# Kernel tuning notes

Measured on AMD Instinct MI355X. Metric: run time of the kernel, lower is better.

Reference implementation:

```python
import jax, jax.numpy as jnp
import numpy as np

B, T, E, H = 2, 2048, 1024, 16
DV = E // H
EPS = 1e-5

def _layernorm(x, g, b):
    m = jnp.mean(x, axis=-1, keepdims=True)
    v = jnp.mean((x - m) ** 2, axis=-1, keepdims=True)
    return (x - m) * jax.lax.rsqrt(v + EPS) * g + b

def setup_inputs() -> dict:
    key = jax.random.key(0)
    ks = jax.random.split(key, 10)
    s = lambda fan_in: 1.0 / np.sqrt(fan_in)
    return {
        "x": jax.random.normal(ks[0], (B, T, E), jnp.float32),
        "wq": jax.random.normal(ks[1], (H, E, DV), jnp.float32) * s(E),
        "wk": jax.random.normal(ks[2], (H, E, DV), jnp.float32) * s(E),
        "wv": jax.random.normal(ks[3], (H, E, DV), jnp.float32) * s(E),
        "w_proj": jax.random.normal(ks[4], (E, E), jnp.float32) * s(E),
        "b_proj": jnp.zeros((E,), jnp.float32),
        "w1": jax.random.normal(ks[5], (E, 4 * E), jnp.float32) * s(E),
        "b1": jnp.zeros((4 * E,), jnp.float32),
        "w2": jax.random.normal(ks[6], (4 * E, E), jnp.float32) * s(4 * E),
        "b2": jnp.zeros((E,), jnp.float32),
        "g1": jnp.ones((E,), jnp.float32),
        "be1": jnp.zeros((E,), jnp.float32),
        "g2": jnp.ones((E,), jnp.float32),
        "be2": jnp.zeros((E,), jnp.float32),
    }

def reference(x, wq, wk, wv, w_proj, b_proj, w1, b1, w2, b2, g1, be1, g2, be2):
    Bc, Tc, C = x.shape
    # --- masked multi-head self-attention on pre-LN input ---
    h = _layernorm(x, g1, be1)
    q = jnp.einsum('bte,hed->bhtd', h, wq)
    k = jnp.einsum('bte,hed->bhtd', h, wk)
    v = jnp.einsum('bte,hed->bhtd', h, wv)
    # NOTE: original scales by C**-0.5 where C = full embed dim (not head dim)
    scores = jnp.einsum('bhtd,bhsd->bhts', q, k) * (C ** -0.5)
    causal = jnp.tril(jnp.ones((Tc, Tc), bool))
    scores = jnp.where(causal, scores, jnp.float32(-jnp.inf))
    probs = jax.nn.softmax(scores, axis=-1)  # dropout is identity in eval
    attn = jnp.einsum('bhts,bhsd->bhtd', probs, v)
    attn = attn.transpose(0, 2, 1, 3).reshape(Bc, Tc, C)
    x = x + (attn @ w_proj + b_proj)
    # --- feed-forward ---
    h2 = _layernorm(x, g2, be2)
    ff = jax.nn.relu(h2 @ w1 + b1) @ w2 + b2
    return x + ff
```

## Files before the change

### kernel.cpp

```cpp
#include <hip/hip_runtime.h>
#include <hip/hip_bf16.h>

typedef __bf16 bf16x8 __attribute__((ext_vector_type(8)));
typedef __bf16 bf16x4 __attribute__((ext_vector_type(4)));
typedef float f32x4 __attribute__((ext_vector_type(4)));

#define T_SEQ 2048
#define EMB 1024
#define NH 16
#define DV 64

__device__ __forceinline__ void gload16(const __bf16* g, __bf16* l) {
    __builtin_amdgcn_global_load_lds(
        (const __attribute__((address_space(1))) unsigned int*)g,
        (__attribute__((address_space(3))) unsigned int*)l, 16, 0, 0);
}

__global__ void transpose_cvt(const float* __restrict__ src, __bf16* __restrict__ dst,
                              int R, int C, long src_bstride, long dst_bstride, float scale) {
    __shared__ float tile[32][33];
    const int b = blockIdx.z;
    const float* s = src + (long)b * src_bstride;
    __bf16* d = dst + (long)b * dst_bstride;
    const int c0 = blockIdx.x * 32, r0 = blockIdx.y * 32;
    #pragma unroll
    for (int i = threadIdx.y; i < 32; i += 8)
        tile[i][threadIdx.x] = s[(long)(r0 + i) * C + c0 + threadIdx.x];
    __syncthreads();
    #pragma unroll
    for (int i = threadIdx.y; i < 32; i += 8)
        d[(long)(c0 + i) * R + r0 + threadIdx.x] = (__bf16)(tile[threadIdx.x][i] * scale);
}

__global__ void vt_transpose(const __bf16* __restrict__ qkv, __bf16* __restrict__ Vt) {
    __shared__ __bf16 tile[64][72];
    const int bh = blockIdx.y, b = bh >> 4, h = bh & 15;
    const int t0 = blockIdx.x * 64;
    const __bf16* src = qkv + (long)b * T_SEQ * 3072 + 2048 + h * 64;
    const int tt = threadIdx.x >> 3, seg = threadIdx.x & 7;
    #pragma unroll
    for (int half = 0; half < 2; half++) {
        const int t = half * 32 + tt;
        bf16x8 v = *reinterpret_cast<const bf16x8*>(src + (long)(t0 + t) * 3072 + seg * 8);
        *reinterpret_cast<bf16x8*>(&tile[t][seg * 8]) = v;
    }
    __syncthreads();
    __bf16* dst = Vt + (long)bh * 64 * T_SEQ + t0;
    #pragma unroll
    for (int half = 0; half < 2; half++) {
        const int d = half * 32 + tt;
        bf16x8 v;
        #pragma unroll
        for (int i = 0; i < 8; i++) v[i] = tile[seg * 8 + i][d];
        *reinterpret_cast<bf16x8*>(dst + (long)d * T_SEQ + seg * 8) = v;
    }
}

__global__ void ln_kernel(const float* __restrict__ x, const float* __restrict__ g,
                          const float* __restrict__ be, __bf16* __restrict__ out) {
    const int row = blockIdx.x;
    const float4 xv = reinterpret_cast<const float4*>(x + (long)row * EMB)[threadIdx.x];
    float s = xv.x + xv.y + xv.z + xv.w;
    float sq = xv.x * xv.x + xv.y * xv.y + xv.z * xv.z + xv.w * xv.w;
    #pragma unroll
    for (int off = 32; off; off >>= 1) { s += __shfl_down(s, off); sq += __shfl_down(sq, off); }
    __shared__ float red[8];
    const int w = threadIdx.x >> 6, lane = threadIdx.x & 63;
    if (lane == 0) { red[w] = s; red[4 + w] = sq; }
    __syncthreads();
    if (threadIdx.x == 0) {
        float st = red[0] + red[1] + red[2] + red[3];
        float sqt = red[4] + red[5] + red[6] + red[7];
        float mean = st * (1.0f / EMB);
        float var = sqt * (1.0f / EMB) - mean * mean;
        red[0] = mean; red[1] = rsqrtf(var + 1e-5f);
    }
    __syncthreads();
    const float mean = red[0], rstd = red[1];
    const float4 gv = reinterpret_cast<const float4*>(g)[threadIdx.x];
    const float4 bv = reinterpret_cast<const float4*>(be)[threadIdx.x];
    bf16x4 o;
    o[0] = (__bf16)((xv.x - mean) * rstd * gv.x + bv.x);
    o[1] = (__bf16)((xv.y - mean) * rstd * gv.y + bv.y);
    o[2] = (__bf16)((xv.z - mean) * rstd * gv.z + bv.z);
    o[3] = (__bf16)((xv.w - mean) * rstd * gv.w + bv.w);
    *reinterpret_cast<bf16x4*>(out + (long)row * EMB + threadIdx.x * 4) = o;
}

template <int BN, int OUT_BF16, int RELU, int HAS_BIAS, int HAS_RES>
__global__ __launch_bounds__(256)
void gemm_nt(const __bf16* __restrict__ A, const __bf16* __restrict__ BT,
             const float* __restrict__ bias, const float* __restrict__ res,
             void* __restrict__ outp, int M, int N, int K) {
    constexpr int NFN = BN / 32;
    __shared__ __align__(16) __bf16 As[128 * 64];
    __shared__ __align__(16) __bf16 Bs[BN * 64];
    const int t = threadIdx.x;
    const int w = t >> 6, lane = t & 63;
    const int wm = (w >> 1) * 64, wn = (w & 1) * (BN / 2);
    const int m0 = blockIdx.y * 128, n0 = blockIdx.x * BN;
    const int rA = lane & 15, kA = (lane >> 4) * 8;
    const int swzr = (rA & 7) * 8;
    const int srow = t >> 3;
    const int chunk = t & 7;
    const int schunk = chunk ^ (srow & 7);

    const __bf16* Ab = A + (long)(m0 + srow) * K + schunk * 8;
    const __bf16* Bb = BT + (long)(n0 + srow) * K + schunk * 8;
    __bf16* Asw = As + srow * 64 + chunk * 8;
    __bf16* Bsw = Bs + srow * 64 + chunk * 8;

    f32x4 acc[4][NFN] = {};
    for (int k0 = 0; k0 < K; k0 += 64) {
        #pragma unroll
        for (int i = 0; i < 4; i++)
            gload16(Ab + (long)(32 * i) * K + k0, Asw + 32 * i * 64);
        #pragma unroll
        for (int i = 0; i < BN / 32; i++)
            gload16(Bb + (long)(32 * i) * K + k0, Bsw + 32 * i * 64);
        __syncthreads();
        #pragma unroll
        for (int kk = 0; kk < 2; kk++) {
            bf16x8 af[4], bfr[NFN];
            #pragma unroll
            for (int m = 0; m < 4; m++)
                af[m] = *reinterpret_cast<const bf16x8*>(
                    As + (wm + m * 16 + rA) * 64 + ((kk * 32 + kA) ^ swzr));
            #pragma unroll
            for (int n = 0; n < NFN; n++)
                bfr[n] = *reinterpret_cast<const bf16x8*>(
                    Bs + (wn + n * 16 + rA) * 64 + ((kk * 32 + kA) ^ swzr));
            #pragma unroll
            for (int m = 0; m < 4; m++)
                #pragma unroll
                for (int n = 0; n < NFN; n++)
                    acc[m][n] = __builtin_amdgcn_mfma_f32_16x16x32_bf16(af[m], bfr[n], acc[m][n], 0, 0, 0);
        }
        __syncthreads();
    }
    const int rl = (lane >> 4) * 4, cl = lane & 15;
    #pragma unroll
    for (int m = 0; m < 4; m++) {
        #pragma unroll
        for (int n = 0; n < NFN; n++) {
            const int gc = n0 + wn + n * 16 + cl;
            float bval = 0.0f;
            if (HAS_BIAS) bval = bias[gc];
            #pragma unroll
            for (int r = 0; r < 4; r++) {
                const int gr = m0 + wm + m * 16 + rl + r;
                float v = acc[m][n][r] + bval;
                if (HAS_RES) v += res[(long)gr * N + gc];
                if (RELU) v = fmaxf(v, 0.0f);
                if (OUT_BF16) ((__bf16*)outp)[(long)gr * N + gc] = (__bf16)v;
                else          ((float*)outp)[(long)gr * N + gc] = v;
            }
        }
    }
}

template <int MASKED>
__device__ __forceinline__ void attn_compute(
    const char* __restrict__ Kl, const char* __restrict__ Vl,
    __bf16 (*__restrict__ PsW)[72],
    const bf16x8 (&qf)[2][2], const bf16x8& ones,
    f32x4 (&o)[2][4], f32x4 (&l5)[2], float (&mr)[2][4],
    int kv0, int rA, int g, int rl, int qw)
{
    const int swz = (rA & 7) << 4;
    bf16x8 kf[4][2];
    #pragma unroll
    for (int c = 0; c < 4; c++)
        #pragma unroll
        for (int kc = 0; kc < 2; kc++)
            kf[c][kc] = *reinterpret_cast<const bf16x8*>(
                Kl + (c * 16 + rA) * 128 + ((kc * 64 + g * 16) ^ swz));
    f32x4 sa[2][4];
    __builtin_amdgcn_s_setprio(1);
    #pragma unroll
    for (int rt = 0; rt < 2; rt++)
        #pragma unroll
        for (int c = 0; c < 4; c++) {
            f32x4 acc = {};
            acc = __builtin_amdgcn_mfma_f32_16x16x32_bf16(qf[rt][0], kf[c][0], acc, 0, 0, 0);
            acc = __builtin_amdgcn_mfma_f32_16x16x32_bf16(qf[rt][1], kf[c][1], acc, 0, 0, 0);
            sa[rt][c] = acc;
        }
    __builtin_amdgcn_s_setprio(0);
    #pragma unroll
    for (int rt = 0; rt < 2; rt++) {
        #pragma unroll
        for (int r = 0; r < 4; r++) {
            float s0 = sa[rt][0][r], s1 = sa[rt][1][r], s2 = sa[rt][2][r], s3 = sa[rt][3][r];
            if (MASKED) {
                const int gr = qw + rt * 16 + rl + r;
                if (kv0 + rA > gr)      s0 = -__builtin_inff();
                if (kv0 + 16 + rA > gr) s1 = -__builtin_inff();
                if (kv0 + 32 + rA > gr) s2 = -__builtin_inff();
                if (kv0 + 48 + rA > gr) s3 = -__builtin_inff();
            }
            float tm = fmaxf(fmaxf(s0, s1), fmaxf(s2, s3));
            #pragma unroll
            for (int msk = 1; msk < 16; msk <<= 1) tm = fmaxf(tm, __shfl_xor(tm, msk));
            const float mo = mr[rt][r];
            float mu = mo;
            if (__any(tm > mo + 8.0f)) {
                const float mn = fmaxf(mo, tm);
                mr[rt][r] = mn;
                const float sc = __expf(mo - mn);
                #pragma unroll
                for (int n = 0; n < 4; n++) o[rt][n][r] *= sc;
                l5[rt][r] *= sc;
                mu = mn;
            }
            const float p0 = __expf(s0 - mu);
            const float p1 = __expf(s1 - mu);
            const float p2 = __expf(s2 - mu);
            const float p3 = __expf(s3 - mu);
            const int prow = rt * 16 + rl + r;
            PsW[prow][rA]      = (__bf16)p0;
            PsW[prow][16 + rA] = (__bf16)p1;
            PsW[prow][32 + rA] = (__bf16)p2;
            PsW[prow][48 + rA] = (__bf16)p3;
        }
    }
    asm volatile("s_waitcnt lgkmcnt(0)" ::: "memory");

    bf16x8 ap[2][2];
    #pragma unroll
    for (int rt = 0; rt < 2; rt++)
        #pragma unroll
        for (int ks = 0; ks < 2; ks++)
            ap[rt][ks] = *reinterpret_cast<const bf16x8*>(&PsW[rt * 16 + rA][ks * 32 + g * 8]);
    __builtin_amdgcn_s_setprio(1);
    #pragma unroll
    for (int ks = 0; ks < 2; ks++) {
        #pragma unroll
        for (int rt = 0; rt < 2; rt++)
            l5[rt] = __builtin_amdgcn_mfma_f32_16x16x32_bf16(ap[rt][ks], ones, l5[rt], 0, 0, 0);
        #pragma unroll
        for (int n = 0; n < 4; n++) {
            bf16x8 bv = *reinterpret_cast<const bf16x8*>(
                Vl + (n * 16 + rA) * 128 + ((ks * 64 + g * 16) ^ swz));
            #pragma unroll
            for (int rt = 0; rt < 2; rt++)
                o[rt][n] = __builtin_amdgcn_mfma_f32_16x16x32_bf16(ap[rt][ks], bv, o[rt][n], 0, 0, 0);
        }
    }
    __builtin_amdgcn_s_setprio(0);
}

__global__ __launch_bounds__(256)
void attn_kernel(const __bf16* __restrict__ qkv, const __bf16* __restrict__ Vt,
                 __bf16* __restrict__ attn) {
    __shared__ __bf16 Ks[2][64 * 64];
    __shared__ __bf16 Vs[2][64 * 64];
    __shared__ __bf16 Ps[4][32][72];

    const int bid = (int)blockIdx.x;
    const int xcd = bid & 7, s = bid >> 3;
    const int slot = s >> 5, c = s & 31;
    const int bh = xcd * 4 + slot * 2 + (c >> 4);
    const int t16 = c & 15;
    const int qtile = slot ? t16 : 15 - t16;
    const int b = bh >> 4, h = bh & 15;
    const int q0 = qtile * 128;
    const int w = threadIdx.x >> 6, lane = threadIdx.x & 63;
    const int qw = q0 + w * 32;
    const int rA = lane & 15, g = lane >> 4, rl = g * 4;
    const int srow8 = lane >> 3;
    const int scol = (lane & 7) * 16;
    const int wcol = scol ^ (srow8 << 4);

    const char* qb = (const char*)(qkv + (long)b * T_SEQ * 3072 + h * 64);
    const char* kb = qb + 2048;
    const char* vtb = (const char*)(Vt + (long)bh * 64 * T_SEQ);

    bf16x8 qf[2][2];
    #pragma unroll
    for (int rt = 0; rt < 2; rt++)
        #pragma unroll
        for (int kc = 0; kc < 2; kc++)
            qf[rt][kc] = *reinterpret_cast<const bf16x8*>(
                qb + (long)(qw + rt * 16 + rA) * 6144 + kc * 64 + g * 16);

    bf16x8 ones;
    #pragma unroll
    for (int i = 0; i < 8; i++) ones[i] = (__bf16)1.0f;

    f32x4 o[2][4] = {};
    f32x4 l5[2] = {};
    float mr[2][4];
    #pragma unroll
    for (int rt = 0; rt < 2; rt++)
        #pragma unroll
        for (int r = 0; r < 4; r++) mr[rt][r] = -__builtin_inff();

    const int nsteps = q0 / 64 + 2;
    const int t_avail = qw + 32;
    const int isK = (w < 2);
    const int r0 = (w & 1) * 32 + srow8;

    bf16x8 stg[4];
    auto issue = [&](int kv0) {
        if (isK) {
            #pragma unroll
            for (int i = 0; i < 4; i++)
                stg[i] = *reinterpret_cast<const bf16x8*>(kb + (long)(kv0 + r0 + i * 8) * 6144 + scol);
        } else {
            #pragma unroll
            for (int i = 0; i < 4; i++)
                stg[i] = *reinterpret_cast<const bf16x8*>(vtb + (long)(r0 + i * 8) * 4096 + kv0 * 2 + scol);
        }
    };
    auto lwrite = [&](int buf) {
        char* base = isK ? (char*)Ks[buf] : (char*)Vs[buf];
        #pragma unroll
        for (int i = 0; i < 4; i++)
            *reinterpret_cast<bf16x8*>(base + (r0 + i * 8) * 128 + wcol) = stg[i];
    };

    issue(0);
    lwrite(0);
    __syncthreads();

    for (int t = 0; t < nsteps; ++t) {
        const int kv0 = t * 64, cur = t & 1;
        const bool has_next = (t + 1 < nsteps);
        if (has_next) issue(kv0 + 64);
        if (kv0 < t_avail) {
            if (kv0 + 64 <= qw)
                attn_compute<0>((const char*)Ks[cur], (const char*)Vs[cur], Ps[w],
                                qf, ones, o, l5, mr, kv0, rA, g, rl, qw);
            else
                attn_compute<1>((const char*)Ks[cur], (const char*)Vs[cur], Ps[w],
                                qf, ones, o, l5, mr, kv0, rA, g, rl, qw);
        }
        if (has_next) lwrite(cur ^ 1);
        __syncthreads();
    }

    #pragma unroll
    for (int rt = 0; rt < 2; rt++)
        #pragma unroll
        for (int n = 0; n < 4; n++)
            #pragma unroll
            for (int r = 0; r < 4; r++) {
                const int gr = qw + rt * 16 + rl + r;
                attn[(long)(b * T_SEQ + gr) * EMB + h * 64 + n * 16 + rA] =
                    (__bf16)(o[rt][n][r] / l5[rt][r]);
            }
}

extern "C" void kernel_launch(void* const* d_in, const int* in_sizes, int n_in,
                              void* d_out, int out_size, void* d_ws, size_t ws_size,
                              hipStream_t stream) {
    const float* x      = (const float*)d_in[0];
    const float* wq     = (const float*)d_in[1];
    const float* wk     = (const float*)d_in[2];
    const float* wv     = (const float*)d_in[3];
    const float* w_proj = (const float*)d_in[4];
    const float* b_proj = (const float*)d_in[5];
    const float* w1     = (const float*)d_in[6];
    const float* b1     = (const float*)d_in[7];
    const float* w2     = (const float*)d_in[8];
    const float* b2     = (const float*)d_in[9];
    const float* g1     = (const float*)d_in[10];
    const float* be1    = (const float*)d_in[11];
    const float* g2     = (const float*)d_in[12];
    const float* be2    = (const float*)d_in[13];
    float* out = (float*)d_out;

    char* ws = (char*)d_ws;
    __bf16* WqkvT = (__bf16*)ws;  ws += 3072L * 1024 * 2;
    __bf16* WprojT = (__bf16*)ws; ws += 1024L * 1024 * 2;
    __bf16* W1T = (__bf16*)ws;    ws += 4096L * 1024 * 2;
    __bf16* W2T = (__bf16*)ws;    ws += 1024L * 4096 * 2;
    __bf16* h1  = (__bf16*)ws;    ws += 4096L * 1024 * 2;
    __bf16* qkvb = (__bf16*)ws;
    __bf16* attnb = (__bf16*)(ws + 4096L * 3072 * 2);
    __bf16* ffb = (__bf16*)ws;    ws += 4096L * 3072 * 2 + 4096L * 1024 * 2;
    float* x2 = (float*)ws;
    __bf16* Vt = (__bf16*)ws;

    const dim3 tb(32, 8);
    transpose_cvt<<<dim3(2, 32, 16), tb, 0, stream>>>(wq, WqkvT,                1024, 64, 65536L, 65536L, 0.03125f);
    transpose_cvt<<<dim3(2, 32, 16), tb, 0, stream>>>(wk, WqkvT + 1024L * 1024, 1024, 64, 65536L, 65536L, 1.0f);
    transpose_cvt<<<dim3(2, 32, 16), tb, 0, stream>>>(wv, WqkvT + 2048L * 1024, 1024, 64, 65536L, 65536L, 1.0f);
    transpose_cvt<<<dim3(32, 32, 1),  tb, 0, stream>>>(w_proj, WprojT, 1024, 1024, 0, 0, 1.0f);
    transpose_cvt<<<dim3(128, 32, 1), tb, 0, stream>>>(w1, W1T, 1024, 4096, 0, 0, 1.0f);
    transpose_cvt<<<dim3(32, 128, 1), tb, 0, stream>>>(w2, W2T, 4096, 1024, 0, 0, 1.0f);

    ln_kernel<<<4096, 256, 0, stream>>>(x, g1, be1, h1);
    gemm_nt<128, 1, 0, 0, 0><<<dim3(24, 32), 256, 0, stream>>>(h1, WqkvT, nullptr, nullptr, qkvb, 4096, 3072, 1024);
    vt_transpose<<<dim3(32, 32), 256, 0, stream>>>(qkvb, Vt);
    attn_kernel<<<512, 256, 0, stream>>>(qkvb, Vt, attnb);
    gemm_nt<64, 0, 0, 1, 1><<<dim3(16, 32), 256, 0, stream>>>(attnb, WprojT, b_proj, x, x2, 4096, 1024, 1024);
    ln_kernel<<<4096, 256, 0, stream>>>(x2, g2, be2, h1);
    gemm_nt<128, 1, 1, 1, 0><<<dim3(32, 32), 256, 0, stream>>>(h1, W1T, b1, nullptr, ffb, 4096, 4096, 1024);
    gemm_nt<64, 0, 0, 1, 1><<<dim3(16, 32), 256, 0, stream>>>(ffb, W2T, b2, x2, out, 4096, 1024, 4096);
}
```

Baseline: 399.7 us.

## Add 256x256 triple-buffered GEMM for QKV and FFN1 projections

Adds a new 512-thread GEMM kernel with 256x256 output tiles, a three-stage LDS ring of direct global-to-LDS loads, swizzled LDS addressing, and an XCD-aware block remap. It replaces the 128-tile GEMM for the QKV projection and the first FFN layer. The goal is more data reuse per tile and better overlap of loads with MFMA work. In exchange the grid gets smaller (192 and 256 blocks), so some CUs may sit idle on the tail, and register pressure rises with the 8x4 accumulator tile. The bf16 epilogue writes scalar stores without coalescing.

Result: faster. 386.6 us (-3.3%).

```diff
diff --git a/kernel.cpp b/kernel.cpp
--- a/kernel.cpp
+++ b/kernel.cpp
@@ -85,6 +85,94 @@
     o[2] = (__bf16)((xv.z - mean) * rstd * gv.z + bv.z);
     o[3] = (__bf16)((xv.w - mean) * rstd * gv.w + bv.w);
     *reinterpret_cast<bf16x4*>(out + (long)row * EMB + threadIdx.x * 4) = o;
+}
+
+template <int RELU, int HAS_BIAS>
+__global__ __launch_bounds__(512)
+void gemm256(const __bf16* __restrict__ A, const __bf16* __restrict__ BT,
+             const float* __restrict__ bias, __bf16* __restrict__ outp,
+             int M, int N, int K, int nbx) {
+    __shared__ __align__(16) __bf16 lds[3][2][256 * 32];
+    const int bid = (int)blockIdx.x;
+    const int cpx = (int)gridDim.x >> 3;
+    const int wg = (bid & 7) * cpx + (bid >> 3);
+    const int bx = wg % nbx, by = wg / nbx;
+    const int m0 = by * 256, n0 = bx * 256;
+    const int tid = threadIdx.x, wid = tid >> 6, lane = tid & 63;
+    const int wr = wid >> 2, wc = wid & 3;
+    const int rA = lane & 15, g = lane >> 4, rl = g * 4;
+    const int rswz = (g ^ ((rA >> 1) & 3)) * 8;
+
+    const int sr = tid >> 2, ch = tid & 3;
+    const int sc = ch ^ ((sr >> 1) & 3);
+    const __bf16* Asrc = A + (long)(m0 + sr) * K + sc * 8;
+    const __bf16* Bsrc = BT + (long)(n0 + sr) * K + sc * 8;
+    const int dOff = sr * 32 + ch * 8;
+
+    auto stage = [&](int t) {
+        const int buf = t % 3, k0 = t * 32;
+        gload16(Asrc + k0,            &lds[buf][0][dOff]);
+        gload16(Asrc + 128 * K + k0,  &lds[buf][0][128 * 32 + dOff]);
+        gload16(Bsrc + k0,            &lds[buf][1][dOff]);
+        gload16(Bsrc + 128 * K + k0,  &lds[buf][1][128 * 32 + dOff]);
+    };
+
+    f32x4 acc[8][4] = {};
+    const int NT = K >> 5;
+    stage(0); stage(1);
+    asm volatile("s_waitcnt vmcnt(4)" ::: "memory");
+    __builtin_amdgcn_s_barrier();
+
+    for (int t = 0; t < NT; ++t) {
+        const int buf = t % 3;
+        if (t + 2 < NT) stage(t + 2);
+        const __bf16* Abuf = lds[buf][0];
+        const __bf16* Bbuf = lds[buf][1];
+        bf16x8 bfr[4], af[8];
+        #pragma unroll
+        for (int n = 0; n < 4; n++)
+            bfr[n] = *reinterpret_cast<const bf16x8*>(Bbuf + (wc * 64 + n * 16 + rA) * 32 + rswz);
+        #pragma unroll
+        for (int m = 0; m < 4; m++)
+            af[m] = *reinterpret_cast<const bf16x8*>(Abuf + (wr * 128 + m * 16 + rA) * 32 + rswz);
+        __builtin_amdgcn_s_setprio(1);
+        #pragma unroll
+        for (int m = 0; m < 4; m++)
+            #pragma unroll
+            for (int n = 0; n < 4; n++)
+                acc[m][n] = __builtin_amdgcn_mfma_f32_16x16x32_bf16(af[m], bfr[n], acc[m][n], 0, 0, 0);
+        __builtin_amdgcn_s_setprio(0);
+        __builtin_amdgcn_s_barrier();
+        #pragma unroll
+        for (int m = 4; m < 8; m++)
+            af[m] = *reinterpret_cast<const bf16x8*>(Abuf + (wr * 128 + m * 16 + rA) * 32 + rswz);
+        __builtin_amdgcn_s_setprio(1);
+        #pragma unroll
+        for (int m = 4; m < 8; m++)
+            #pragma unroll
+            for (int n = 0; n < 4; n++)
+                acc[m][n] = __builtin_amdgcn_mfma_f32_16x16x32_bf16(af[m], bfr[n], acc[m][n], 0, 0, 0);
+        __builtin_amdgcn_s_setprio(0);
+        asm volatile("s_waitcnt vmcnt(4)" ::: "memory");
+        __builtin_amdgcn_s_barrier();
+    }
+
+    #pragma unroll
+    for (int m = 0; m < 8; m++) {
+        #pragma unroll
+        for (int n = 0; n < 4; n++) {
+            const int gc = n0 + wc * 64 + n * 16 + rA;
+            float bval = 0.0f;
+            if (HAS_BIAS) bval = bias[gc];
+            #pragma unroll
+            for (int r = 0; r < 4; r++) {
+                const int gr = m0 + wr * 128 + m * 16 + rl + r;
+                float v = acc[m][n][r] + bval;
+                if (RELU) v = fmaxf(v, 0.0f);
+                outp[(long)gr * N + gc] = (__bf16)v;
+            }
+        }
+    }
 }
 
 template <int BN, int OUT_BF16, int RELU, int HAS_BIAS, int HAS_RES>
@@ -392,11 +480,11 @@
     transpose_cvt<<<dim3(32, 128, 1), tb, 0, stream>>>(w2, W2T, 4096, 1024, 0, 0, 1.0f);
 
     ln_kernel<<<4096, 256, 0, stream>>>(x, g1, be1, h1);
-    gemm_nt<128, 1, 0, 0, 0><<<dim3(24, 32), 256, 0, stream>>>(h1, WqkvT, nullptr, nullptr, qkvb, 4096, 3072, 1024);
+    gemm256<0, 0><<<192, 512, 0, stream>>>(h1, WqkvT, nullptr, qkvb, 4096, 3072, 1024, 12);
     vt_transpose<<<dim3(32, 32), 256, 0, stream>>>(qkvb, Vt);
     attn_kernel<<<512, 256, 0, stream>>>(qkvb, Vt, attnb);
     gemm_nt<64, 0, 0, 1, 1><<<dim3(16, 32), 256, 0, stream>>>(attnb, WprojT, b_proj, x, x2, 4096, 1024, 1024);
     ln_kernel<<<4096, 256, 0, stream>>>(x2, g2, be2, h1);
-    gemm_nt<128, 1, 1, 1, 0><<<dim3(32, 32), 256, 0, stream>>>(h1, W1T, b1, nullptr, ffb, 4096, 4096, 1024);
+    gemm256<1, 1><<<256, 512, 0, stream>>>(h1, W1T, b1, ffb, 4096, 4096, 1024, 16);
     gemm_nt<64, 0, 0, 1, 1><<<dim3(16, 32), 256, 0, stream>>>(ffb, W2T, b2, x2, out, 4096, 1024, 4096);
 }
```
